# Performance work log

Hardware: AMD Instinct MI355X
Metric: run time of the kernel (lower is better)

The kernel has to match this reference:

```python
import jax, jax.numpy as jnp
import numpy as np

B, T, I, H = 32768, 512, 2, 16  # batch, seq_len, input_size, hidden_size


def setup_inputs() -> dict:
    key = jax.random.key(0)
    ks = jax.random.split(key, 9)
    sc_i = 1.0 / np.sqrt(H)  # torch LSTM/Linear init scale ~ U(-1/sqrt(H), 1/sqrt(H)); use normal*scale
    return {
        "x": jax.random.normal(ks[0], (B, T, I), jnp.float32),
        "W_ih": jax.random.normal(ks[1], (4 * H, I), jnp.float32) * sc_i,
        "W_hh": jax.random.normal(ks[2], (4 * H, H), jnp.float32) * sc_i,
        "b_ih": jax.random.normal(ks[3], (4 * H,), jnp.float32) * sc_i,
        "b_hh": jax.random.normal(ks[4], (4 * H,), jnp.float32) * sc_i,
        "W1": jax.random.normal(ks[5], (H, H), jnp.float32) * sc_i,
        "b1": jax.random.normal(ks[6], (H,), jnp.float32) * sc_i,
        "W2": jax.random.normal(ks[7], (I, H), jnp.float32) * sc_i,
        "b2": jax.random.normal(ks[8], (I,), jnp.float32) * sc_i,
    }


def reference(x, W_ih, W_hh, b_ih, b_hh, W1, b1, W2, b2):
    # x: [B, T, I]. torch forward permutes to (T, B, I) and runs seq-first LSTM.
    # Precompute input projections for all timesteps (one big GEMM): [B, T, 4H]
    x_proj = jnp.einsum('bti,gi->btg', x, W_ih) + b_ih + b_hh
    Whh_T = W_hh.T  # [H, 4H]

    def step(carry, xt):
        h, c = carry                      # [B, H] each
        gates = xt + h @ Whh_T            # [B, 4H]
        i, f, g, o = jnp.split(gates, 4, axis=-1)  # torch gate order: i, f, g, o
        i = jax.nn.sigmoid(i)
        f = jax.nn.sigmoid(f)
        g = jnp.tanh(g)
        o = jax.nn.sigmoid(o)
        c = f * c + i * g
        h = o * jnp.tanh(c)
        return (h, c), None

    bsz = x.shape[0]
    h0 = jnp.zeros((bsz, W_hh.shape[1]), x.dtype)
    c0 = jnp.zeros_like(h0)
    (h_last, _), _ = jax.lax.scan(step, (h0, c0), jnp.swapaxes(x_proj, 0, 1))
    # MLP head on last hidden state: Linear -> tanh -> Linear
    y = jnp.tanh(h_last @ W1.T + b1) @ W2.T + b2  # [B, I]
    return y
```

## Files before the change

### kernel.cpp

```cpp
#include <hip/hip_runtime.h>


#define T_STEPS 512
#define LOG2E 1.44269504088896340736f

typedef __bf16 bf16x8 __attribute__((ext_vector_type(8)));
typedef float  f32x4  __attribute__((ext_vector_type(4)));
typedef float  f32x2  __attribute__((ext_vector_type(2)));
typedef unsigned int u32x4 __attribute__((ext_vector_type(4)));

union frag_u { u32x4 u; bf16x8 v; };

#if __has_builtin(__builtin_amdgcn_exp2f)
__device__ __forceinline__ float fexp2(float x) { return __builtin_amdgcn_exp2f(x); }
#else
__device__ __forceinline__ float fexp2(float x) { return exp2f(x); }
#endif
#if __has_builtin(__builtin_amdgcn_rcpf)
__device__ __forceinline__ float frcp(float x) { return __builtin_amdgcn_rcpf(x); }
#else
__device__ __forceinline__ float frcp(float x) { return 1.0f / x; }
#endif

__device__ __forceinline__ f32x2 vexp2(f32x2 a) { f32x2 r; r.x = fexp2(a.x); r.y = fexp2(a.y); return r; }
__device__ __forceinline__ f32x2 vrcp (f32x2 a) { f32x2 r; r.x = frcp(a.x);  r.y = frcp(a.y);  return r; }

__device__ __forceinline__ unsigned dup_hi(float h) {
    unsigned hb = __float_as_uint(h);
#if __has_builtin(__builtin_amdgcn_perm)
    return __builtin_amdgcn_perm(hb, hb, 0x03020302u);
#else
    return (hb >> 16) | (hb & 0xFFFF0000u);
#endif
}
__device__ __forceinline__ unsigned lo_part(float h) {
    unsigned hb = __float_as_uint(h);
    float    res = h - __uint_as_float(hb & 0xFFFF0000u);
    return __float_as_uint(res) >> 16;
}
__device__ __forceinline__ unsigned pack_hilo(float h) {
    unsigned hb = __float_as_uint(h);
    float    res = h - __uint_as_float(hb & 0xFFFF0000u);
#if __has_builtin(__builtin_amdgcn_perm)
    return __builtin_amdgcn_perm(__float_as_uint(res), hb, 0x07060302u);
#else
    return (hb >> 16) | (__float_as_uint(res) & 0xFFFF0000u);
#endif
}

__global__ __launch_bounds__(256, 2)
void lstm_mfma_kernel(const float* __restrict__ x,
                      const float* __restrict__ W_ih,
                      const float* __restrict__ W_hh,
                      const float* __restrict__ b_ih,
                      const float* __restrict__ b_hh,
                      const float* __restrict__ W1,
                      const float* __restrict__ b1,
                      const float* __restrict__ W2,
                      const float* __restrict__ b2,
                      float* __restrict__ out)
{
    __shared__ float hsm[4][16][16];

    const int tid  = threadIdx.x;
    const int wv   = tid >> 6;
    const int lane = tid & 63;
    const int e    = lane & 15;
    const int q    = lane >> 4;

    const float gsc[4] = { -LOG2E, -LOG2E, 2.0f * LOG2E, -LOG2E };

    frag_u A1[4];
    #pragma unroll
    for (int t = 0; t < 4; ++t) {
        const int row = 16 * t + (lane & 15);
        const float4 w4 = *(const float4*)(W_hh + row * 16 + 4 * q);
        A1[t].u[0] = pack_hilo(w4.x * gsc[t]);
        A1[t].u[1] = pack_hilo(w4.y * gsc[t]);
        A1[t].u[2] = pack_hilo(w4.z * gsc[t]);
        A1[t].u[3] = pack_hilo(w4.w * gsc[t]);
    }

    f32x2 wx2[4][2], wy2[4][2], bs2[4][2];
    #pragma unroll
    for (int t = 0; t < 4; ++t)
        #pragma unroll
        for (int p = 0; p < 2; ++p) {
            const int r0 = 16 * t + 4 * q + 2 * p;
            const int r1 = r0 + 1;
            wx2[t][p].x = W_ih[r0 * 2 + 0] * gsc[t];
            wx2[t][p].y = W_ih[r1 * 2 + 0] * gsc[t];
            wy2[t][p].x = W_ih[r0 * 2 + 1] * gsc[t];
            wy2[t][p].y = W_ih[r1 * 2 + 1] * gsc[t];
            bs2[t][p].x = (b_ih[r0] + b_hh[r0]) * gsc[t];
            bs2[t][p].y = (b_ih[r1] + b_hh[r1]) * gsc[t];
        }

    const int gelem = blockIdx.x * 64 + wv * 16 + e;
    const float4* xp = (const float4*)(x + (size_t)gelem * (T_STEPS * 2));

    frag_u Bh, Bl;
    #pragma unroll
    for (int w = 0; w < 4; ++w) { Bh.u[w] = 0u; Bl.u[w] = 0u; }
    f32x2 cs2[2];
    cs2[0] = 0.0f; cs2[1] = 0.0f;

    float4 xv = xp[0];

    for (int t2 = 0; t2 < T_STEPS / 2; ++t2) {
        const float4 xnext = xp[(t2 + 1) & (T_STEPS / 2 - 1)];

        f32x4 ini[2][4];
        #pragma unroll
        for (int half = 0; half < 2; ++half) {
            const float xa = half ? xv.z : xv.x;
            const float xb = half ? xv.w : xv.y;
            #pragma unroll
            for (int t = 0; t < 4; ++t)
                #pragma unroll
                for (int p = 0; p < 2; ++p) {
                    f32x2 v = wy2[t][p] * xb + bs2[t][p];
                    v = wx2[t][p] * xa + v;
                    ini[half][t][2 * p]     = v.x;
                    ini[half][t][2 * p + 1] = v.y;
                }
        }

        #pragma unroll
        for (int half = 0; half < 2; ++half) {
            f32x4 acc[4];
            #pragma unroll
            for (int t = 0; t < 4; ++t) {
                acc[t] = __builtin_amdgcn_mfma_f32_16x16x32_bf16(A1[t].v, Bh.v, ini[half][t], 0, 0, 0);
                acc[t] = __builtin_amdgcn_mfma_f32_16x16x32_bf16(A1[t].v, Bl.v, acc[t], 0, 0, 0);
            }

            #pragma unroll
            for (int p = 0; p < 2; ++p) {
                f32x2 aI, aF, aG, aO;
                aI.x = acc[0][2 * p]; aI.y = acc[0][2 * p + 1];
                aF.x = acc[1][2 * p]; aF.y = acc[1][2 * p + 1];
                aG.x = acc[2][2 * p]; aG.y = acc[2][2 * p + 1];
                aO.x = acc[3][2 * p]; aO.y = acc[3][2 * p + 1];

                const f32x2 I = vexp2(aI), F = vexp2(aF);
                const f32x2 G = vexp2(aG), O = vexp2(aO);

                const f32x2 Ip = I + 1.0f, Gp = G + 1.0f;
                const f32x2 Fp = F + 1.0f, Op = O + 1.0f;

                const f32x2 P1 = Ip * Gp;
                const f32x2 P2 = Fp * Op;
                const f32x2 R  = vrcp(P1 * P2);

                const f32x2 Gm   = G * (2.0f * LOG2E) + (-2.0f * LOG2E);
                const f32x2 t_sf = P1 * Op;
                const f32x2 t_so = P1 * Fp;
                const f32x2 t_ig = Gm * P2;

                const f32x2 u1 = t_sf * cs2[p] + t_ig;
                cs2[p] = u1 * R;

                const f32x2 C2 = vexp2(cs2[p]);
                const f32x2 Rd = vrcp(C2 + 1.0f);
                const f32x2 tc = Rd * (-2.0f) + 1.0f;
                const f32x2 so = t_so * R;
                const f32x2 hn = so * tc;

                Bh.u[2 * p]     = dup_hi(hn.x);
                Bh.u[2 * p + 1] = dup_hi(hn.y);
                Bl.u[2 * p]     = lo_part(hn.x);
                Bl.u[2 * p + 1] = lo_part(hn.y);
            }
        }
        xv = xnext;
    }

    #pragma unroll
    for (int r = 0; r < 4; ++r) {
        const float hval = __uint_as_float(Bh.u[r] << 16) +
                           __uint_as_float(Bl.u[r] << 16);
        hsm[wv][e][4 * q + r] = hval;
    }

    float hv[16];
    #pragma unroll
    for (int j = 0; j < 4; ++j) {
        const float4 t4 = *(const float4*)&hsm[wv][e][4 * j];
        hv[4 * j + 0] = t4.x; hv[4 * j + 1] = t4.y;
        hv[4 * j + 2] = t4.z; hv[4 * j + 3] = t4.w;
    }

    float z[4];
    #pragma unroll
    for (int r = 0; r < 4; ++r) {
        const int m = 4 * q + r;
        float a = b1[m];
        #pragma unroll
        for (int j = 0; j < 16; ++j) a = fmaf(W1[m * 16 + j], hv[j], a);
        const float E = fexp2(a * (2.0f * LOG2E));
        z[r] = fmaf(-2.0f, frcp(1.0f + E), 1.0f);
    }
    #pragma unroll
    for (int r = 0; r < 4; ++r) hsm[wv][e][4 * q + r] = z[r];

    if (q < 2) {
        float a = b2[q];
        #pragma unroll
        for (int j = 0; j < 16; ++j) a = fmaf(W2[q * 16 + j], hsm[wv][e][j], a);
        out[(size_t)gelem * 2 + q] = a;
    }
}

extern "C" void kernel_launch(void* const* d_in, const int* in_sizes, int n_in,
                              void* d_out, int out_size, void* d_ws, size_t ws_size,
                              hipStream_t stream) {
    const float* x    = (const float*)d_in[0];
    const float* W_ih = (const float*)d_in[1];
    const float* W_hh = (const float*)d_in[2];
    const float* b_ih = (const float*)d_in[3];
    const float* b_hh = (const float*)d_in[4];
    const float* W1   = (const float*)d_in[5];
    const float* b1   = (const float*)d_in[6];
    const float* W2   = (const float*)d_in[7];
    const float* b2   = (const float*)d_in[8];
    float* out = (float*)d_out;

    lstm_mfma_kernel<<<dim3(512), dim3(256), 0, stream>>>(
        x, W_ih, W_hh, b_ih, b_hh, W1, b1, W2, b2, out);
}
```

Before: 488.0 us.

## Fold input projection into MFMA operand and permute gate rows per lane

Packs the bf16 hi/lo split of x_t into unused K slots of the low-part B fragment, with matching W_ih columns in a second A fragment. The input projection is then computed by the MFMA instead of per-step VALU FMAs. Gate rows are permuted so each lane's accumulator holds i,f,g,o for one hidden unit, which removes the cross-accumulator shuffles. The recurrence is ping-ponged between two fragment sets. The risks are the correctness of the new element mapping and the precision of packing x into bf16 hi/lo pairs.

```diff
diff --git a/kernel.cpp b/kernel.cpp
--- a/kernel.cpp
+++ b/kernel.cpp
@@ -22,9 +22,6 @@
 __device__ __forceinline__ float frcp(float x) { return 1.0f / x; }
 #endif
 
-__device__ __forceinline__ f32x2 vexp2(f32x2 a) { f32x2 r; r.x = fexp2(a.x); r.y = fexp2(a.y); return r; }
-__device__ __forceinline__ f32x2 vrcp (f32x2 a) { f32x2 r; r.x = frcp(a.x);  r.y = frcp(a.y);  return r; }
-
 __device__ __forceinline__ unsigned dup_hi(float h) {
     unsigned hb = __float_as_uint(h);
 #if __has_builtin(__builtin_amdgcn_perm)
@@ -33,10 +30,12 @@
     return (hb >> 16) | (hb & 0xFFFF0000u);
 #endif
 }
-__device__ __forceinline__ unsigned lo_part(float h) {
-    unsigned hb = __float_as_uint(h);
-    float    res = h - __uint_as_float(hb & 0xFFFF0000u);
-    return __float_as_uint(res) >> 16;
+__device__ __forceinline__ unsigned lo_with_x(float res, unsigned xq) {
+#if __has_builtin(__builtin_amdgcn_perm)
+    return __builtin_amdgcn_perm(xq, __float_as_uint(res), 0x07060302u);
+#else
+    return (__float_as_uint(res) >> 16) | (xq & 0xFFFF0000u);
+#endif
 }
 __device__ __forceinline__ unsigned pack_hilo(float h) {
     unsigned hb = __float_as_uint(h);
@@ -46,6 +45,55 @@
 #else
     return (hb >> 16) | (__float_as_uint(res) & 0xFFFF0000u);
 #endif
+}
+__device__ __forceinline__ unsigned bfhi(float v) {
+    return __float_as_uint(v) & 0xFFFF0000u;
+}
+__device__ __forceinline__ unsigned make_xq(float nx0, float nx1, int q) {
+    const float xs = (q & 2) ? nx1 : nx0;
+    const unsigned h16 = bfhi(xs);
+    const unsigned l16 = bfhi(xs - __uint_as_float(h16));
+    return (q & 1) ? l16 : h16;
+}
+
+__device__ __forceinline__ void lstm_step(
+    const frag_u& BhI, const frag_u& BlI,
+    frag_u& BhO, frag_u& BlO,
+    float cs[4],
+    const frag_u A1[4], const frag_u A2[4], const f32x4 biasf[4],
+    unsigned xqn)
+{
+    f32x4 acc[4];
+    #pragma unroll
+    for (int t = 0; t < 4; ++t)
+        acc[t] = __builtin_amdgcn_mfma_f32_16x16x32_bf16(A1[t].v, BhI.v, biasf[t], 0, 0, 0);
+
+    #pragma unroll
+    for (int t = 0; t < 4; ++t) {
+        acc[t] = __builtin_amdgcn_mfma_f32_16x16x32_bf16(A2[t].v, BlI.v, acc[t], 0, 0, 0);
+
+        f32x2 eIF, eGO;
+        eIF.x = fexp2(acc[t][0]);
+        eIF.y = fexp2(acc[t][1]);
+        eGO.x = fexp2(acc[t][2]);
+        eGO.y = fexp2(acc[t][3]);
+        const f32x2 pA = eIF + 1.0f;
+        const f32x2 pB = eGO + 1.0f;
+        const f32x2 PP = pA * pB;
+        const float R  = frcp(PP.x * PP.y);
+        const float Gm = fmaf(2.0f * LOG2E, eGO.x, -2.0f * LOG2E);
+        const float u1 = fmaf(PP.x * pB.y, cs[t], Gm * PP.y);
+        const float csn = u1 * R;
+        cs[t] = csn;
+        const float C2 = fexp2(csn);
+        const float tc = fmaf(-2.0f, frcp(C2 + 1.0f), 1.0f);
+        const float hn = (PP.x * pA.y) * R * tc;
+
+        const unsigned hb = __float_as_uint(hn);
+        BhO.u[t] = dup_hi(hn);
+        const float resf = hn - __uint_as_float(hb & 0xFFFF0000u);
+        BlO.u[t] = lo_with_x(resf, xqn);
+    }
 }
 
 __global__ __launch_bounds__(256, 2)
@@ -67,120 +115,74 @@
     const int lane = tid & 63;
     const int e    = lane & 15;
     const int q    = lane >> 4;
+    const int m    = lane & 15;
 
     const float gsc[4] = { -LOG2E, -LOG2E, 2.0f * LOG2E, -LOG2E };
 
-    frag_u A1[4];
+    frag_u A1[4], A2[4];
+    f32x4  biasf[4];
     #pragma unroll
     for (int t = 0; t < 4; ++t) {
-        const int row = 16 * t + (lane & 15);
-        const float4 w4 = *(const float4*)(W_hh + row * 16 + 4 * q);
-        A1[t].u[0] = pack_hilo(w4.x * gsc[t]);
-        A1[t].u[1] = pack_hilo(w4.y * gsc[t]);
-        A1[t].u[2] = pack_hilo(w4.z * gsc[t]);
-        A1[t].u[3] = pack_hilo(w4.w * gsc[t]);
-    }
-
-    f32x2 wx2[4][2], wy2[4][2], bs2[4][2];
-    #pragma unroll
-    for (int t = 0; t < 4; ++t)
-        #pragma unroll
-        for (int p = 0; p < 2; ++p) {
-            const int r0 = 16 * t + 4 * q + 2 * p;
-            const int r1 = r0 + 1;
-            wx2[t][p].x = W_ih[r0 * 2 + 0] * gsc[t];
-            wx2[t][p].y = W_ih[r1 * 2 + 0] * gsc[t];
-            wy2[t][p].x = W_ih[r0 * 2 + 1] * gsc[t];
-            wy2[t][p].y = W_ih[r1 * 2 + 1] * gsc[t];
-            bs2[t][p].x = (b_ih[r0] + b_hh[r0]) * gsc[t];
-            bs2[t][p].y = (b_ih[r1] + b_hh[r1]) * gsc[t];
+        const int   g  = m & 3;
+        const int   Rr = g * 16 + 4 * t + (m >> 2);
+        const float sc = gsc[g];
+
+        const float xw0 = W_ih[Rr * 2 + 0] * sc;
+        const float xw1 = W_ih[Rr * 2 + 1] * sc;
+        const unsigned x0h = bfhi(xw0);
+        const unsigned x0l = bfhi(xw0 - __uint_as_float(x0h));
+        const unsigned x1h = bfhi(xw1);
+        const unsigned x1l = bfhi(xw1 - __uint_as_float(x1h));
+        const unsigned cw0 = (q < 2) ? x0h : x1h;
+        const unsigned cw1 = (q < 2) ? x0l : x1l;
+
+        #pragma unroll
+        for (int w = 0; w < 4; ++w) {
+            const float whh = W_hh[Rr * 16 + 4 * w + q] * sc;
+            A1[t].u[w] = pack_hilo(whh);
+            A2[t].u[w] = __float_as_uint(whh) >> 16;
         }
+        A2[t].u[0] |= cw0;
+        A2[t].u[1] |= cw1;
+
+        #pragma unroll
+        for (int j = 0; j < 4; ++j) {
+            const int Rb = j * 16 + 4 * t + q;
+            biasf[t][j] = (b_ih[Rb] + b_hh[Rb]) * gsc[j];
+        }
+    }
 
     const int gelem = blockIdx.x * 64 + wv * 16 + e;
     const float4* xp = (const float4*)(x + (size_t)gelem * (T_STEPS * 2));
 
-    frag_u Bh, Bl;
-    #pragma unroll
-    for (int w = 0; w < 4; ++w) { Bh.u[w] = 0u; Bl.u[w] = 0u; }
-    f32x2 cs2[2];
-    cs2[0] = 0.0f; cs2[1] = 0.0f;
+    frag_u BhA, BlA, BhB, BlB;
+    float  cs[4] = {0.f, 0.f, 0.f, 0.f};
 
     float4 xv = xp[0];
+
+    {
+        const unsigned xq0 = make_xq(xv.x, xv.y, q);
+        #pragma unroll
+        for (int w = 0; w < 4; ++w) { BhA.u[w] = 0u; BlA.u[w] = xq0; }
+    }
 
     for (int t2 = 0; t2 < T_STEPS / 2; ++t2) {
         const float4 xnext = xp[(t2 + 1) & (T_STEPS / 2 - 1)];
 
-        f32x4 ini[2][4];
-        #pragma unroll
-        for (int half = 0; half < 2; ++half) {
-            const float xa = half ? xv.z : xv.x;
-            const float xb = half ? xv.w : xv.y;
-            #pragma unroll
-            for (int t = 0; t < 4; ++t)
-                #pragma unroll
-                for (int p = 0; p < 2; ++p) {
-                    f32x2 v = wy2[t][p] * xb + bs2[t][p];
-                    v = wx2[t][p] * xa + v;
-                    ini[half][t][2 * p]     = v.x;
-                    ini[half][t][2 * p + 1] = v.y;
-                }
-        }
-
-        #pragma unroll
-        for (int half = 0; half < 2; ++half) {
-            f32x4 acc[4];
-            #pragma unroll
-            for (int t = 0; t < 4; ++t) {
-                acc[t] = __builtin_amdgcn_mfma_f32_16x16x32_bf16(A1[t].v, Bh.v, ini[half][t], 0, 0, 0);
-                acc[t] = __builtin_amdgcn_mfma_f32_16x16x32_bf16(A1[t].v, Bl.v, acc[t], 0, 0, 0);
-            }
-
-            #pragma unroll
-            for (int p = 0; p < 2; ++p) {
-                f32x2 aI, aF, aG, aO;
-                aI.x = acc[0][2 * p]; aI.y = acc[0][2 * p + 1];
-                aF.x = acc[1][2 * p]; aF.y = acc[1][2 * p + 1];
-                aG.x = acc[2][2 * p]; aG.y = acc[2][2 * p + 1];
-                aO.x = acc[3][2 * p]; aO.y = acc[3][2 * p + 1];
-
-                const f32x2 I = vexp2(aI), F = vexp2(aF);
-                const f32x2 G = vexp2(aG), O = vexp2(aO);
-
-                const f32x2 Ip = I + 1.0f, Gp = G + 1.0f;
-                const f32x2 Fp = F + 1.0f, Op = O + 1.0f;
-
-                const f32x2 P1 = Ip * Gp;
-                const f32x2 P2 = Fp * Op;
-                const f32x2 R  = vrcp(P1 * P2);
-
-                const f32x2 Gm   = G * (2.0f * LOG2E) + (-2.0f * LOG2E);
-                const f32x2 t_sf = P1 * Op;
-                const f32x2 t_so = P1 * Fp;
-                const f32x2 t_ig = Gm * P2;
-
-                const f32x2 u1 = t_sf * cs2[p] + t_ig;
-                cs2[p] = u1 * R;
-
-                const f32x2 C2 = vexp2(cs2[p]);
-                const f32x2 Rd = vrcp(C2 + 1.0f);
-                const f32x2 tc = Rd * (-2.0f) + 1.0f;
-                const f32x2 so = t_so * R;
-                const f32x2 hn = so * tc;
-
-                Bh.u[2 * p]     = dup_hi(hn.x);
-                Bh.u[2 * p + 1] = dup_hi(hn.y);
-                Bl.u[2 * p]     = lo_part(hn.x);
-                Bl.u[2 * p + 1] = lo_part(hn.y);
-            }
-        }
+        const unsigned xq1 = make_xq(xv.z, xv.w, q);
+        const unsigned xq2 = make_xq(xnext.x, xnext.y, q);
+
+        lstm_step(BhA, BlA, BhB, BlB, cs, A1, A2, biasf, xq1);
+        lstm_step(BhB, BlB, BhA, BlA, cs, A1, A2, biasf, xq2);
+
         xv = xnext;
     }
 
     #pragma unroll
     for (int r = 0; r < 4; ++r) {
-        const float hval = __uint_as_float(Bh.u[r] << 16) +
-                           __uint_as_float(Bl.u[r] << 16);
-        hsm[wv][e][4 * q + r] = hval;
+        const float hval = __uint_as_float(BhA.u[r] << 16) +
+                           __uint_as_float(BlA.u[r] << 16);
+        hsm[wv][e][4 * r + q] = hval;
     }
 
     float hv[16];
@@ -194,10 +196,10 @@
     float z[4];
     #pragma unroll
     for (int r = 0; r < 4; ++r) {
-        const int m = 4 * q + r;
-        float a = b1[m];
-        #pragma unroll
-        for (int j = 0; j < 16; ++j) a = fmaf(W1[m * 16 + j], hv[j], a);
+        const int mm = 4 * q + r;
+        float a = b1[mm];
+        #pragma unroll
+        for (int j = 0; j < 16; ++j) a = fmaf(W1[mm * 16 + j], hv[j], a);
         const float E = fexp2(a * (2.0f * LOG2E));
         z[r] = fmaf(-2.0f, frcp(1.0f + E), 1.0f);
     }
```

New measurement: 497.0 us, median of 2. No clear change (+1.8%).
